# Kernel optimization log

Hardware: AMD Instinct MI355X
Metric: run time of the kernel (lower is better)

Reference implementation:

```python
import math
import jax, jax.numpy as jnp
import numpy as np

H = 8  # h_heads (init kwarg)
D = 512  # d_hiddens
N, S = 4, 1024  # batch, seq (q == s assumed by the module's mask construction)
NEG = -1.0e9


def setup_inputs() -> dict:
    key = jax.random.key(0)
    ks = jax.random.split(key, 13)
    scale = 1.0 / math.sqrt(D)
    inp = {
        "queries_nqd": jax.random.normal(ks[0], (N, S, D), jnp.float32),
        "keys_nsd": jax.random.normal(ks[1], (N, S, D), jnp.float32),
        "values_nsd": jax.random.normal(ks[2], (N, S, D), jnp.float32),
        "prefix_len_n": jax.random.randint(ks[3], (N,), 0, S),
        "Wq": jax.random.normal(ks[4], (D, D), jnp.float32) * scale,
        "bq": jnp.zeros((D,), jnp.float32),
        "Wk": jax.random.normal(ks[5], (D, D), jnp.float32) * scale,
        "bk": jnp.zeros((D,), jnp.float32),
        "Wv": jax.random.normal(ks[6], (D, D), jnp.float32) * scale,
        "bv": jnp.zeros((D,), jnp.float32),
        "Wo": jax.random.normal(ks[7], (D, D), jnp.float32) * scale,
        "bo": jnp.zeros((D,), jnp.float32),
    }
    return inp


def _split_heads(x_nqd):
    n, q, d = x_nqd.shape
    return x_nqd.reshape(n, q, H, d // H).transpose(0, 2, 1, 3).reshape(n * H, q, d // H)


def _merge_heads(x_mqk):
    m, q, dh = x_mqk.shape
    return x_mqk.reshape(m // H, H, q, dh).transpose(0, 2, 1, 3).reshape(m // H, q, H * dh)


def reference(queries_nqd, keys_nsd, values_nsd, prefix_len_n, Wq, bq, Wk, bk, Wv, bv, Wo, bo):
    q_nqd = queries_nqd @ Wq.T + bq
    k_nsd = keys_nsd @ Wk.T + bk
    v_nsd = values_nsd @ Wv.T + bv

    q_mqk = _split_heads(q_nqd)   # [n*H, s, dh]
    k_msk = _split_heads(k_nsd)
    v_msk = _split_heads(v_nsd)
    prefix_m = jnp.repeat(prefix_len_n, H)  # per-head prefix, n-major to match split_heads

    dh = q_mqk.shape[-1]
    s = k_msk.shape[1]
    scores_mqs = jnp.einsum("mqd,msd->mqs", q_mqk, k_msk) / math.sqrt(dh)

    col = jnp.arange(s)
    block_mask = col[None, None, :] < prefix_m[:, None, None]        # [m,1,s] -> bcast [m,s,s]
    diag_mask = jnp.eye(s, dtype=bool)[None, :, :]                    # [1,s,s]
    attn_mask = block_mask | diag_mask                                # True = attend

    scores_mqs = jnp.where(attn_mask, scores_mqs, NEG)
    probs_mqs = jax.nn.softmax(scores_mqs, axis=-1)  # dropout p=0.0 -> identity
    out_mqk = jnp.einsum("mqs,msd->mqd", probs_mqs, v_msk)

    out_nqd = _merge_heads(out_mqk)
    return out_nqd @ Wo.T + bo
```

## Files before the change

kernel.cpp:

```cpp
#include <hip/hip_runtime.h>
#include <hip/hip_bf16.h>


typedef short bf16x8 __attribute__((ext_vector_type(8)));
typedef float f32x4 __attribute__((ext_vector_type(4)));
typedef int   i32x4 __attribute__((ext_vector_type(4)));
typedef unsigned short u16;
typedef unsigned int   u32;

#define MFMA_BF16(A, B, C) __builtin_amdgcn_mfma_f32_16x16x32_bf16((A), (B), (C), 0, 0, 0)

typedef const __attribute__((address_space(1))) void gv_t;
typedef __attribute__((address_space(3))) void lv_t;

__device__ __forceinline__ u16 cvt_bf16(float f) {
    return __builtin_bit_cast(u16, __float2bfloat16(f));
}
__device__ __forceinline__ u32 cvt2(float lo, float hi) {
    return (u32)cvt_bf16(lo) | ((u32)cvt_bf16(hi) << 16);
}

__global__ __launch_bounds__(256) void prep_kernel(
    const float* __restrict__ xq, const float* __restrict__ xk, const float* __restrict__ xv,
    const float* __restrict__ wq, const float* __restrict__ wk, const float* __restrict__ wv,
    const float* __restrict__ wo,
    u16* __restrict__ xqb, u16* __restrict__ xkb, u16* __restrict__ xvb,
    u16* __restrict__ wqb, u16* __restrict__ wkb, u16* __restrict__ wvb,
    u16* __restrict__ wob) {
    const int z = blockIdx.y;
    const float* src;
    u16* dst;
    int nblk;
    switch (z) {
        case 0: src = xq; dst = xqb; nblk = 1024; break;
        case 1: src = xk; dst = xkb; nblk = 1024; break;
        case 2: src = xv; dst = xvb; nblk = 1024; break;
        case 3: src = wq; dst = wqb; nblk = 128; break;
        case 4: src = wk; dst = wkb; nblk = 128; break;
        case 5: src = wv; dst = wvb; nblk = 128; break;
        default: src = wo; dst = wob; nblk = 128; break;
    }
    if (blockIdx.x >= (unsigned)nblk) return;
    size_t i = ((size_t)blockIdx.x * 256 + threadIdx.x) * 8;
    f32x4 a = *reinterpret_cast<const f32x4*>(src + i);
    f32x4 b = *reinterpret_cast<const f32x4*>(src + i + 4);
    i32x4 p;
    p[0] = cvt2(a[0], a[1]); p[1] = cvt2(a[2], a[3]);
    p[2] = cvt2(b[0], b[1]); p[3] = cvt2(b[2], b[3]);
    *reinterpret_cast<i32x4*>(dst + i) = p;
}

template <int OMODE>
__device__ __forceinline__ void gemm_bf(const u16* __restrict__ X,
                                        const u16* __restrict__ W,
                                        const float* __restrict__ bias,
                                        void* __restrict__ out_, float scale) {
    extern __shared__ char smem[];

    const int tid = threadIdx.x;
    const int m0 = blockIdx.x * 128;
    const int n0 = blockIdx.y * 64;
    const int w = tid >> 6, l = tid & 63;
    const int wm = (w >> 1) * 64, wn = (w & 1) * 32;
    const int lg = l >> 4, lr = l & 15;

    const int row8 = l >> 3;
    const int slotg = (l & 7) ^ row8;
    const u16* gA = X + (size_t)(m0 + w * 32 + row8) * 512 + slotg * 8;
    const u16* gB = W + (size_t)(n0 + w * 16 + row8) * 512 + slotg * 8;

    f32x4 acc[4][2];
#pragma unroll
    for (int i = 0; i < 4; i++)
#pragma unroll
        for (int j = 0; j < 2; j++) acc[i][j] = (f32x4){0.f, 0.f, 0.f, 0.f};

    auto STAGE = [&](int t, int buf) {
        char* As = smem + buf * 24576;
        char* Bs = As + 16384;
        const int k0 = t * 64;
#pragma unroll
        for (int c = 0; c < 4; c++)
            __builtin_amdgcn_global_load_lds((gv_t*)(gA + c * 8 * 512 + k0),
                                             (lv_t*)(As + (w * 4 + c) * 1024), 16, 0, 0);
#pragma unroll
        for (int c = 0; c < 2; c++)
            __builtin_amdgcn_global_load_lds((gv_t*)(gB + c * 8 * 512 + k0),
                                             (lv_t*)(Bs + (w * 2 + c) * 1024), 16, 0, 0);
    };
    auto COMPUTE = [&](int buf) {
        char* As = smem + buf * 24576;
        char* Bs = As + 16384;
#pragma unroll
        for (int kk = 0; kk < 2; kk++) {
            bf16x8 af[4], bfr[2];
#pragma unroll
            for (int i = 0; i < 4; i++) {
                int ra_ = wm + i * 16 + lr;
                af[i] = *reinterpret_cast<const bf16x8*>(
                    As + ra_ * 128 + ((kk * 64 + lg * 16) ^ ((ra_ & 7) << 4)));
            }
#pragma unroll
            for (int j = 0; j < 2; j++) {
                int rb_ = wn + j * 16 + lr;
                bfr[j] = *reinterpret_cast<const bf16x8*>(
                    Bs + rb_ * 128 + ((kk * 64 + lg * 16) ^ ((rb_ & 7) << 4)));
            }
            __builtin_amdgcn_s_setprio(1);
#pragma unroll
            for (int i = 0; i < 4; i++)
#pragma unroll
                for (int j = 0; j < 2; j++) acc[i][j] = MFMA_BF16(af[i], bfr[j], acc[i][j]);
            __builtin_amdgcn_s_setprio(0);
        }
    };

    STAGE(0, 0);
    __syncthreads();
    int buf = 0;
#pragma unroll
    for (int t = 0; t < 8; ++t) {
        if (t < 7) STAGE(t + 1, buf ^ 1);
        COMPUTE(buf);
        __syncthreads();
        buf ^= 1;
    }

#pragma unroll
    for (int j = 0; j < 2; j++) {
        int col = n0 + wn + j * 16 + lr;
        float bc_ = bias[col];
#pragma unroll
        for (int i = 0; i < 4; i++) {
            int grbase = m0 + wm + i * 16 + lg * 4;
            if (OMODE == 0) {
                float* out = (float*)out_;
#pragma unroll
                for (int r = 0; r < 4; r++)
                    out[(size_t)(grbase + r) * 512 + col] = (acc[i][j][r] + bc_) * scale;
            } else if (OMODE == 1) {
                u16* out = (u16*)out_;
#pragma unroll
                for (int r = 0; r < 4; r++)
                    out[(size_t)(grbase + r) * 512 + col] = cvt_bf16((acc[i][j][r] + bc_) * scale);
            } else {
                u16* out = (u16*)out_;
                int mh = ((grbase >> 10) * 8) + (col >> 6);
                int t2 = grbase & 1023;
                u32 p0 = cvt2((acc[i][j][0] + bc_) * scale, (acc[i][j][1] + bc_) * scale);
                u32 p1 = cvt2((acc[i][j][2] + bc_) * scale, (acc[i][j][3] + bc_) * scale);
                u32* dst = reinterpret_cast<u32*>(out + ((size_t)mh * 64 + (col & 63)) * 1024 + t2);
                dst[0] = p0;
                dst[1] = p1;
            }
        }
    }
}

__global__ __launch_bounds__(256) void qkv_gemm(
    const u16* __restrict__ Xq, const u16* __restrict__ Xk, const u16* __restrict__ Xv,
    const u16* __restrict__ Wq, const u16* __restrict__ Wk, const u16* __restrict__ Wv,
    const float* __restrict__ bq, const float* __restrict__ bk, const float* __restrict__ bv,
    u16* __restrict__ Qb, u16* __restrict__ Kb, u16* __restrict__ Vt) {
    int z = blockIdx.z;
    if (z == 0)      gemm_bf<1>(Xq, Wq, bq, Qb, 0.125f);
    else if (z == 1) gemm_bf<1>(Xk, Wk, bk, Kb, 1.0f);
    else             gemm_bf<2>(Xv, Wv, bv, Vt, 1.0f);
}

__global__ __launch_bounds__(256) void out_gemm(const u16* __restrict__ AO,
                                                const u16* __restrict__ Wo,
                                                const float* __restrict__ bo,
                                                float* __restrict__ out) {
    gemm_bf<0>(AO, Wo, bo, out, 1.0f);
}

__global__ __launch_bounds__(256) void attn_kernel(const u16* __restrict__ Qb,
                                                   const u16* __restrict__ Kb,
                                                   const u16* __restrict__ Vt,
                                                   const int* __restrict__ prefix,
                                                   u16* __restrict__ AO) {
    const int tid = threadIdx.x;
    const int w = tid >> 6, l = tid & 63;
    const int lg = l >> 4, lr = l & 15;
    const int qblk = blockIdx.x;
    const int m = blockIdx.y;
    const int n = m >> 3, h = m & 7;
    const int q0 = qblk * 64 + w * 16;
    const int P = prefix[n];

    const u16* qptr = Qb + (size_t)(n * 1024 + q0 + lr) * 512 + h * 64 + lg * 8;
    bf16x8 qf0 = *reinterpret_cast<const bf16x8*>(qptr);
    bf16x8 qf1 = *reinterpret_cast<const bf16x8*>(qptr + 32);

    f32x4 o[4];
#pragma unroll
    for (int j = 0; j < 4; j++) o[j] = (f32x4){0.f, 0.f, 0.f, 0.f};
    float mrow = -1.0e9f, lsum = 0.f;

    const int T = (P + 31) >> 5;
    const int dt = q0 >> 5;
    const int nt = T + ((dt >= T) ? 1 : 0);
    const int q_glob = q0 + lr;
    const f32x4 fz = (f32x4){0.f, 0.f, 0.f, 0.f};

    const u16* kbase = Kb + (size_t)(n * 1024 + lr) * 512 + h * 64 + lg * 8;
    const u16* vbase = Vt + ((size_t)m * 64 + lr) * 1024 + lg * 8;

    struct KV { bf16x8 k0, k1, k2, k3, v0, v1, v2, v3; };

    auto s0_of = [&](int it) { return ((it < T) ? it : dt) << 5; };
    auto LOADKV = [&](int s0, KV& t) {
        const u16* kp = kbase + (size_t)s0 * 512;
        t.k0 = *reinterpret_cast<const bf16x8*>(kp);
        t.k1 = *reinterpret_cast<const bf16x8*>(kp + 32);
        t.k2 = *reinterpret_cast<const bf16x8*>(kp + 16 * 512);
        t.k3 = *reinterpret_cast<const bf16x8*>(kp + 16 * 512 + 32);
        const u16* vp = vbase + s0;
        t.v0 = *reinterpret_cast<const bf16x8*>(vp);
        t.v1 = *reinterpret_cast<const bf16x8*>(vp + 16 * 1024);
        t.v2 = *reinterpret_cast<const bf16x8*>(vp + 32 * 1024);
        t.v3 = *reinterpret_cast<const bf16x8*>(vp + 48 * 1024);
    };
    auto STEP = [&](int s0, const KV& t) {
        f32x4 st[2];
        __builtin_amdgcn_s_setprio(1);
        st[0] = MFMA_BF16(t.k0, qf0, fz);
        st[0] = MFMA_BF16(t.k1, qf1, st[0]);
        st[1] = MFMA_BF16(t.k2, qf0, fz);
        st[1] = MFMA_BF16(t.k3, qf1, st[1]);
        __builtin_amdgcn_s_setprio(0);

#pragma unroll
        for (int c = 0; c < 2; c++)
#pragma unroll
            for (int r = 0; r < 4; r++) {
                int s = s0 + c * 16 + lg * 4 + r;
                float v = fminf(st[c][r], 1.0e4f);
                st[c][r] = ((s < P) || (s == q_glob)) ? v : -1.0e9f;
            }

        float tm = st[0][0];
#pragma unroll
        for (int r = 1; r < 4; r++) tm = fmaxf(tm, st[0][r]);
#pragma unroll
        for (int r = 0; r < 4; r++) tm = fmaxf(tm, st[1][r]);
        tm = fmaxf(tm, __shfl_xor(tm, 16));
        tm = fmaxf(tm, __shfl_xor(tm, 32));
        float Mn = fmaxf(mrow, tm);
        float alpha = __expf(mrow - Mn);
        float ts = 0.f;
#pragma unroll
        for (int c = 0; c < 2; c++)
#pragma unroll
            for (int r = 0; r < 4; r++) {
                float p = __expf(st[c][r] - Mn);
                st[c][r] = p;
                ts += p;
            }
        ts += __shfl_xor(ts, 16);
        ts += __shfl_xor(ts, 32);
        lsum = lsum * alpha + ts;
        mrow = Mn;

        float a4[4];
#pragma unroll
        for (int r = 0; r < 4; r++) a4[r] = __shfl(alpha, lg * 4 + r);
#pragma unroll
        for (int j = 0; j < 4; j++) {
            o[j][0] *= a4[0]; o[j][1] *= a4[1]; o[j][2] *= a4[2]; o[j][3] *= a4[3];
        }

        u32 pk[2][2];
#pragma unroll
        for (int c = 0; c < 2; c++) {
            pk[c][0] = cvt2(st[c][0], st[c][1]);
            pk[c][1] = cvt2(st[c][2], st[c][3]);
        }
        i32x4 pav;
#pragma unroll
        for (int wd = 0; wd < 4; wd++) {
            int src = ((2 * (lg & 1) + (wd >> 1)) << 4) + lr;
            int t0 = __shfl((int)pk[0][wd & 1], src);
            int t1 = __shfl((int)pk[1][wd & 1], src);
            pav[wd] = (lg >> 1) ? t1 : t0;
        }
        bf16x8 paf = __builtin_bit_cast(bf16x8, pav);

        __builtin_amdgcn_s_setprio(1);
        o[0] = MFMA_BF16(paf, t.v0, o[0]);
        o[1] = MFMA_BF16(paf, t.v1, o[1]);
        o[2] = MFMA_BF16(paf, t.v2, o[2]);
        o[3] = MFMA_BF16(paf, t.v3, o[3]);
        __builtin_amdgcn_s_setprio(0);
    };

    KV A_, B_;
    LOADKV(s0_of(0), A_);
    for (int it = 0; it < nt; it += 2) {
        if (it + 1 < nt) LOADKV(s0_of(it + 1), B_);
        STEP(s0_of(it), A_);
        if (it + 1 >= nt) break;
        if (it + 2 < nt) LOADKV(s0_of(it + 2), A_);
        STEP(s0_of(it + 1), B_);
    }

    float linv = 1.0f / fmaxf(lsum, 1.0e-30f);
    float li[4];
#pragma unroll
    for (int r = 0; r < 4; r++) li[r] = __shfl(linv, lg * 4 + r);

    u16* obase = AO + (size_t)(n * 1024 + q0 + lg * 4) * 512 + h * 64 + lr;
#pragma unroll
    for (int j = 0; j < 4; j++)
#pragma unroll
        for (int r = 0; r < 4; r++) {
            float v = fminf(fmaxf(o[j][r] * li[r], -1.0e4f), 1.0e4f);
            obase[(size_t)r * 512 + j * 16] = cvt_bf16(v);
        }
}

extern "C" void kernel_launch(void* const* d_in, const int* in_sizes, int n_in,
                              void* d_out, int out_size, void* d_ws, size_t ws_size,
                              hipStream_t stream) {
    (void)in_sizes; (void)n_in; (void)out_size;
    const float* queries = (const float*)d_in[0];
    const float* keys    = (const float*)d_in[1];
    const float* values  = (const float*)d_in[2];
    const int*   prefix  = (const int*)d_in[3];
    const float* Wq = (const float*)d_in[4];
    const float* bq = (const float*)d_in[5];
    const float* Wk = (const float*)d_in[6];
    const float* bk = (const float*)d_in[7];
    const float* Wv = (const float*)d_in[8];
    const float* bv = (const float*)d_in[9];
    const float* Wo = (const float*)d_in[10];
    const float* bo = (const float*)d_in[11];
    float* outp = (float*)d_out;

    const size_t XEL = (size_t)4096 * 512;
    const size_t WEL = (size_t)512 * 512;
    size_t need = (3 * XEL + 4 * WEL + 4 * XEL) * sizeof(u16);
    if (ws_size < need) return;
    u16* Xqb = (u16*)d_ws;
    u16* Xkb = Xqb + XEL;
    u16* Xvb = Xkb + XEL;
    u16* Wqb = Xvb + XEL;
    u16* Wkb = Wqb + WEL;
    u16* Wvb = Wkb + WEL;
    u16* Wob = Wvb + WEL;
    u16* Qb  = Wob + WEL;
    u16* Kb  = Qb + XEL;
    u16* Vt  = Kb + XEL;
    u16* AO  = Vt + XEL;

    dim3 blk(256);
    prep_kernel<<<dim3(1024, 7), blk, 0, stream>>>(queries, keys, values, Wq, Wk, Wv, Wo,
                                                   Xqb, Xkb, Xvb, Wqb, Wkb, Wvb, Wob);
    const int SMEM = 49152;
    qkv_gemm<<<dim3(32, 8, 3), blk, SMEM, stream>>>(Xqb, Xkb, Xvb, Wqb, Wkb, Wvb,
                                                    bq, bk, bv, Qb, Kb, Vt);
    attn_kernel<<<dim3(16, 32), blk, 0, stream>>>(Qb, Kb, Vt, prefix, AO);
    out_gemm<<<dim3(32, 8, 1), blk, SMEM, stream>>>(AO, Wob, bo, outp);
}
```

Baseline: 59.15 us.

## Widen attention KV tiles to 64, skip full-tile masking, defer softmax rescale

```diff
diff --git a/kernel.cpp b/kernel.cpp
--- a/kernel.cpp
+++ b/kernel.cpp
@@ -106,12 +106,10 @@
                 bfr[j] = *reinterpret_cast<const bf16x8*>(
                     Bs + rb_ * 128 + ((kk * 64 + lg * 16) ^ ((rb_ & 7) << 4)));
             }
-            __builtin_amdgcn_s_setprio(1);
 #pragma unroll
             for (int i = 0; i < 4; i++)
 #pragma unroll
                 for (int j = 0; j < 2; j++) acc[i][j] = MFMA_BF16(af[i], bfr[j], acc[i][j]);
-            __builtin_amdgcn_s_setprio(0);
         }
     };
 
@@ -198,8 +196,8 @@
     for (int j = 0; j < 4; j++) o[j] = (f32x4){0.f, 0.f, 0.f, 0.f};
     float mrow = -1.0e9f, lsum = 0.f;
 
-    const int T = (P + 31) >> 5;
-    const int dt = q0 >> 5;
+    const int T = (P + 63) >> 6;
+    const int dt = qblk;
     const int nt = T + ((dt >= T) ? 1 : 0);
     const int q_glob = q0 + lr;
     const f32x4 fz = (f32x4){0.f, 0.f, 0.f, 0.f};
@@ -207,51 +205,57 @@
     const u16* kbase = Kb + (size_t)(n * 1024 + lr) * 512 + h * 64 + lg * 8;
     const u16* vbase = Vt + ((size_t)m * 64 + lr) * 1024 + lg * 8;
 
-    struct KV { bf16x8 k0, k1, k2, k3, v0, v1, v2, v3; };
-
-    auto s0_of = [&](int it) { return ((it < T) ? it : dt) << 5; };
+    struct KV { bf16x8 k[4][2]; bf16x8 v[4][2]; };
+
+    auto s0_of = [&](int it) { return ((it < T) ? it : dt) << 6; };
     auto LOADKV = [&](int s0, KV& t) {
-        const u16* kp = kbase + (size_t)s0 * 512;
-        t.k0 = *reinterpret_cast<const bf16x8*>(kp);
-        t.k1 = *reinterpret_cast<const bf16x8*>(kp + 32);
-        t.k2 = *reinterpret_cast<const bf16x8*>(kp + 16 * 512);
-        t.k3 = *reinterpret_cast<const bf16x8*>(kp + 16 * 512 + 32);
+#pragma unroll
+        for (int c = 0; c < 4; c++) {
+            const u16* kp = kbase + (size_t)(s0 + c * 16) * 512;
+            t.k[c][0] = *reinterpret_cast<const bf16x8*>(kp);
+            t.k[c][1] = *reinterpret_cast<const bf16x8*>(kp + 32);
+        }
         const u16* vp = vbase + s0;
-        t.v0 = *reinterpret_cast<const bf16x8*>(vp);
-        t.v1 = *reinterpret_cast<const bf16x8*>(vp + 16 * 1024);
-        t.v2 = *reinterpret_cast<const bf16x8*>(vp + 32 * 1024);
-        t.v3 = *reinterpret_cast<const bf16x8*>(vp + 48 * 1024);
+#pragma unroll
+        for (int j = 0; j < 4; j++) {
+            t.v[j][0] = *reinterpret_cast<const bf16x8*>(vp + (size_t)j * 16 * 1024);
+            t.v[j][1] = *reinterpret_cast<const bf16x8*>(vp + (size_t)j * 16 * 1024 + 32);
+        }
     };
     auto STEP = [&](int s0, const KV& t) {
-        f32x4 st[2];
+        f32x4 st[4];
         __builtin_amdgcn_s_setprio(1);
-        st[0] = MFMA_BF16(t.k0, qf0, fz);
-        st[0] = MFMA_BF16(t.k1, qf1, st[0]);
-        st[1] = MFMA_BF16(t.k2, qf0, fz);
-        st[1] = MFMA_BF16(t.k3, qf1, st[1]);
+#pragma unroll
+        for (int c = 0; c < 4; c++) {
+            st[c] = MFMA_BF16(t.k[c][0], qf0, fz);
+            st[c] = MFMA_BF16(t.k[c][1], qf1, st[c]);
+        }
         __builtin_amdgcn_s_setprio(0);
 
-#pragma unroll
-        for (int c = 0; c < 2; c++)
-#pragma unroll
-            for (int r = 0; r < 4; r++) {
-                int s = s0 + c * 16 + lg * 4 + r;
-                float v = fminf(st[c][r], 1.0e4f);
-                st[c][r] = ((s < P) || (s == q_glob)) ? v : -1.0e9f;
-            }
+        if (s0 + 64 > P) {
+#pragma unroll
+            for (int c = 0; c < 4; c++)
+#pragma unroll
+                for (int r = 0; r < 4; r++) {
+                    int s = s0 + c * 16 + lg * 4 + r;
+                    if (!((s < P) || (s == q_glob))) st[c][r] = -1.0e9f;
+                }
+        }
 
         float tm = st[0][0];
 #pragma unroll
-        for (int r = 1; r < 4; r++) tm = fmaxf(tm, st[0][r]);
-#pragma unroll
-        for (int r = 0; r < 4; r++) tm = fmaxf(tm, st[1][r]);
+        for (int c = 0; c < 4; c++)
+#pragma unroll
+            for (int r = 0; r < 4; r++) tm = fmaxf(tm, st[c][r]);
         tm = fmaxf(tm, __shfl_xor(tm, 16));
         tm = fmaxf(tm, __shfl_xor(tm, 32));
-        float Mn = fmaxf(mrow, tm);
-        float alpha = __expf(mrow - Mn);
+
+        const bool defer = __all(tm - mrow <= 8.0f);
+        const float Mn = defer ? mrow : fmaxf(mrow, tm);
+
         float ts = 0.f;
 #pragma unroll
-        for (int c = 0; c < 2; c++)
+        for (int c = 0; c < 4; c++)
 #pragma unroll
             for (int r = 0; r < 4; r++) {
                 float p = __expf(st[c][r] - Mn);
@@ -260,38 +264,47 @@
             }
         ts += __shfl_xor(ts, 16);
         ts += __shfl_xor(ts, 32);
-        lsum = lsum * alpha + ts;
-        mrow = Mn;
-
-        float a4[4];
-#pragma unroll
-        for (int r = 0; r < 4; r++) a4[r] = __shfl(alpha, lg * 4 + r);
-#pragma unroll
-        for (int j = 0; j < 4; j++) {
-            o[j][0] *= a4[0]; o[j][1] *= a4[1]; o[j][2] *= a4[2]; o[j][3] *= a4[3];
-        }
-
-        u32 pk[2][2];
-#pragma unroll
-        for (int c = 0; c < 2; c++) {
+
+        if (defer) {
+            lsum += ts;
+        } else {
+            float alpha = __expf(mrow - Mn);
+            lsum = lsum * alpha + ts;
+            mrow = Mn;
+            float a4[4];
+#pragma unroll
+            for (int r = 0; r < 4; r++) a4[r] = __shfl(alpha, lg * 4 + r);
+#pragma unroll
+            for (int j = 0; j < 4; j++) {
+                o[j][0] *= a4[0]; o[j][1] *= a4[1]; o[j][2] *= a4[2]; o[j][3] *= a4[3];
+            }
+        }
+
+        u32 pk[4][2];
+#pragma unroll
+        for (int c = 0; c < 4; c++) {
             pk[c][0] = cvt2(st[c][0], st[c][1]);
             pk[c][1] = cvt2(st[c][2], st[c][3]);
         }
-        i32x4 pav;
+        i32x4 pav0, pav1;
 #pragma unroll
         for (int wd = 0; wd < 4; wd++) {
             int src = ((2 * (lg & 1) + (wd >> 1)) << 4) + lr;
-            int t0 = __shfl((int)pk[0][wd & 1], src);
-            int t1 = __shfl((int)pk[1][wd & 1], src);
-            pav[wd] = (lg >> 1) ? t1 : t0;
-        }
-        bf16x8 paf = __builtin_bit_cast(bf16x8, pav);
+            int a0 = __shfl((int)pk[0][wd & 1], src);
+            int a1 = __shfl((int)pk[1][wd & 1], src);
+            pav0[wd] = (lg >> 1) ? a1 : a0;
+            int b0 = __shfl((int)pk[2][wd & 1], src);
+            int b1 = __shfl((int)pk[3][wd & 1], src);
+            pav1[wd] = (lg >> 1) ? b1 : b0;
+        }
+        bf16x8 paf0 = __builtin_bit_cast(bf16x8, pav0);
+        bf16x8 paf1 = __builtin_bit_cast(bf16x8, pav1);
 
         __builtin_amdgcn_s_setprio(1);
-        o[0] = MFMA_BF16(paf, t.v0, o[0]);
-        o[1] = MFMA_BF16(paf, t.v1, o[1]);
-        o[2] = MFMA_BF16(paf, t.v2, o[2]);
-        o[3] = MFMA_BF16(paf, t.v3, o[3]);
+#pragma unroll
+        for (int j = 0; j < 4; j++) o[j] = MFMA_BF16(paf0, t.v[j][0], o[j]);
+#pragma unroll
+        for (int j = 0; j < 4; j++) o[j] = MFMA_BF16(paf1, t.v[j][1], o[j]);
         __builtin_amdgcn_s_setprio(0);
     };
 
@@ -340,7 +353,7 @@
 
     const size_t XEL = (size_t)4096 * 512;
     const size_t WEL = (size_t)512 * 512;
-    size_t need = (3 * XEL + 4 * WEL + 4 * XEL) * sizeof(u16);
+    size_t need = (7 * XEL + 4 * WEL) * sizeof(u16);
     if (ws_size < need) return;
     u16* Xqb = (u16*)d_ws;
     u16* Xkb = Xqb + XEL;
```

After: 61.96 us. +4.8%, slower.
